# Performance work log

Measured on AMD Instinct MI355X. Metric: run time of the kernel, lower is better.

## Reference

```python
import jax, jax.numpy as jnp
import numpy as np
from jax import lax

ALPHA = float(np.exp(-1.0 / 5.0))   # exp(-1/tau_mem), tau_mem=5.0
THRESHOLD = 1.0


def _dwconv(x, w, b, groups):
    # x: (B, Cin, T), w: (Cout, Cin/groups, K), 'same' padding for odd K
    pad = (w.shape[-1] - 1) // 2
    y = lax.conv_general_dilated(
        x, w, window_strides=(1,), padding=[(pad, pad)],
        dimension_numbers=("NCH", "OIH", "NCH"), feature_group_count=groups)
    return y + b[None, :, None]


def setup_inputs() -> dict:
    key = jax.random.key(0)
    ks = jax.random.split(key, 12)
    B, C, T = 8, 256, 4096
    OP = 6            # out_per_kernel for each of the 3 kernel sizes
    DEC = 128         # decoder_channels
    f32 = jnp.float32
    d = {}
    d["x"] = jax.random.normal(ks[0], (B, C, T), f32)
    # depthwise multi-path conv params (groups=C): weight (C*OP, 1, K)
    d["w3"] = jax.random.normal(ks[1], (C * OP, 1, 3), f32) * 0.2
    d["b3"] = jnp.zeros((C * OP,), f32)
    d["w5"] = jax.random.normal(ks[2], (C * OP, 1, 5), f32) * 0.15
    d["b5"] = jnp.zeros((C * OP,), f32)
    d["w9"] = jax.random.normal(ks[3], (C * OP, 1, 9), f32) * 0.1
    d["b9"] = jnp.zeros((C * OP,), f32)
    # reduce: Conv1d(C*18 -> C, k=1, groups=C): weight (C, 18, 1)
    d["w_red"] = jax.random.normal(ks[4], (C, 3 * OP, 1), f32) * 0.2
    d["b_red"] = jnp.zeros((C,), f32)
    d["latency_scale"] = jnp.asarray(5.0, f32)
    # output_gates: xavier uniform (C, C) with zero diagonal
    bound = float(np.sqrt(6.0 / (C + C)))
    og = jax.random.uniform(ks[5], (C, C), f32, -bound, bound)
    d["output_gates"] = og * (1.0 - jnp.eye(C, dtype=f32))
    d["bias"] = jnp.zeros((C,), f32)
    # post_mlp: Linear(C, DEC) -> ReLU -> Linear(DEC, C); stored as (in, out)
    d["W1"] = jax.random.normal(ks[6], (C, DEC), f32) * float(np.sqrt(2.0 / C))
    d["b1"] = jnp.zeros((DEC,), f32)
    d["W2"] = jax.random.normal(ks[7], (DEC, C), f32) * float(np.sqrt(2.0 / DEC))
    d["b2"] = jnp.zeros((C,), f32)
    return d


def reference(x, w3, b3, w5, b5, w9, b9, w_red, b_red,
              latency_scale, output_gates, bias, W1, b1, W2, b2):
    B, C, T = x.shape
    # DepthwiseMultiPathEncoder: 3 depthwise convs -> cat -> grouped 1x1 reduce
    o3 = _dwconv(x, w3, b3, C)
    o5 = _dwconv(x, w5, b5, C)
    o9 = _dwconv(x, w9, b9, C)
    cat = jnp.concatenate([o3, o5, o9], axis=1)      # (B, 18C, T)
    drive = _dwconv(cat, w_red, b_red, C)             # (B, C, T)
    # LIF membrane recurrence + first-spike latency (sequential over T)
    d_t = jnp.moveaxis(drive, 2, 0)                   # (T, B, C)
    def step(V, dt):
        V = ALPHA * V + (1.0 - ALPHA) * dt
        return V, V >= THRESHOLD
    _, crossed = lax.scan(step, jnp.zeros((B, C), x.dtype), d_t)  # (T, B, C) bool
    fired_any = crossed.any(axis=0)
    first_t = jnp.argmax(crossed, axis=0)             # first True index
    true_latency = jnp.where(fired_any, first_t, T).astype(x.dtype)  # (B, C)
    # latency -> activation -> gated mix -> MLP -> softplus, clamp [0, T]
    scale = jnp.maximum(latency_scale, 0.001)
    act = jnp.exp(-true_latency / scale)              # (B, C)
    mixed = act @ output_gates.T + bias[None, :]      # (B, C)
    h = jax.nn.relu(mixed @ W1 + b1)
    raw_pred = h @ W2 + b2
    pred_latency = jnp.clip(jax.nn.softplus(raw_pred), 0.0, float(T))
    return pred_latency, true_latency, act
```

## Files before the change

kernel.cpp:

```cpp
#include <hip/hip_runtime.h>
#include <math.h>

#define C_CH 256
#define T_LEN 4096


template <int K>
__device__ inline void fold_bundle(const float* __restrict__ wp,
                                   const float* __restrict__ bp,
                                   const float* __restrict__ wred6,
                                   int p0, float* __restrict__ w9,
                                   float& bacc, int& src)
{
    const int off = (9 - K) >> 1;
    src = p0 / 6;
    #pragma unroll
    for (int k = 0; k < 9; ++k) w9[k] = 0.0f;
    #pragma unroll
    for (int j = 0; j < 6; ++j) {
        const float wr = wred6[j];
        bacc += wr * bp[p0 + j];
        #pragma unroll
        for (int k = 0; k < K; ++k)
            w9[off + k] += wr * wp[(p0 + j) * K + k];
    }
}

__global__ __launch_bounds__(256) void fold_kernel(
    const float* __restrict__ w3, const float* __restrict__ b3,
    const float* __restrict__ w5, const float* __restrict__ b5,
    const float* __restrict__ w9, const float* __restrict__ b9,
    const float* __restrict__ w_red, const float* __restrict__ b_red,
    float* __restrict__ ws)
{
    const int c = threadIdx.x;
    float wf[3][9];
    int   src[3];
    float bacc = 0.0f;
    #pragma unroll
    for (int r = 0; r < 3; ++r) {
        const int q0 = 18 * c + 6 * r;
        const float* wred6 = w_red + c * 18 + 6 * r;
        if (q0 < 1536)      fold_bundle<3>(w3, b3, wred6, q0,        wf[r], bacc, src[r]);
        else if (q0 < 3072) fold_bundle<5>(w5, b5, wred6, q0 - 1536, wf[r], bacc, src[r]);
        else                fold_bundle<9>(w9, b9, wred6, q0 - 3072, wf[r], bacc, src[r]);
    }
    float* o = ws + c * 32;
    #pragma unroll
    for (int r = 0; r < 3; ++r)
        #pragma unroll
        for (int k = 0; k < 9; ++k) o[r * 9 + k] = wf[r][k];
    o[27] = b_red[c] + bacc;
    #pragma unroll
    for (int r = 0; r < 3; ++r) ((int*)o)[28 + r] = src[r];
    o[31] = 0.0f;
}

__global__ __launch_bounds__(256) void drive_scan_kernel(
    const float* __restrict__ x,
    const float* __restrict__ ws,
    const float* __restrict__ latency_scale,
    float* __restrict__ out_lat, float* __restrict__ out_act)
{
    const int blk  = blockIdx.x;
    const int b    = blk >> 8;
    const int c    = blk & 255;
    const int tid  = threadIdx.x;
    const int lane = tid & 63;
    const int wv   = tid >> 6;

    __shared__ float sWS[32];
    __shared__ float sWaveTot[4];
    __shared__ float sCarry[4];
    __shared__ int   sMin[4];

    if (tid < 32) sWS[tid] = ws[c * 32 + tid];
    __syncthreads();

    const float A   = (float)0.8187307530779818;
    const float OMA = (float)(1.0 - 0.8187307530779818);
    const float Beff = sWS[27];

    float d[16];
    #pragma unroll
    for (int tt = 0; tt < 16; ++tt) d[tt] = Beff;

    const int i    = tid;
    const int base = 16 * i - 4;
    #pragma unroll
    for (int r = 0; r < 3; ++r) {
        const int srcc = ((const int*)sWS)[28 + r];
        const float* xr = x + ((size_t)b * C_CH + srcc) * T_LEN;
        float xa[24];
        if (i > 0 && i < 255) {
            const float4* p = (const float4*)(xr + base);
            #pragma unroll
            for (int v = 0; v < 6; ++v) {
                float4 q = p[v];
                xa[4 * v + 0] = q.x; xa[4 * v + 1] = q.y;
                xa[4 * v + 2] = q.z; xa[4 * v + 3] = q.w;
            }
        } else {
            #pragma unroll
            for (int e = 0; e < 24; ++e) {
                const int t = base + e;
                xa[e] = (t >= 0 && t < T_LEN) ? xr[t] : 0.0f;
            }
        }
        float wk[9];
        #pragma unroll
        for (int k = 0; k < 9; ++k) wk[k] = sWS[r * 9 + k];
        #pragma unroll
        for (int tt = 0; tt < 16; ++tt) {
            #pragma unroll
            for (int k = 0; k < 9; ++k)
                d[tt] = fmaf(wk[k], xa[tt + k], d[tt]);
        }
    }

    float S = 0.0f;
    #pragma unroll
    for (int tt = 0; tt < 16; ++tt) S = A * S + OMA * d[tt];

    const float Fp[6] = {
        (float)4.0762203978366215e-02,
        (float)1.6615572731739337e-03,
        (float)2.7607725720371943e-06,
        (float)7.6218649302532563e-12,
        (float)5.8092835977683129e-23,
        (float)3.3744728758705166e-45
    };
    float cinc = S;
    #pragma unroll
    for (int s = 0; s < 6; ++s) {
        const int o = 1 << s;
        const float y = __shfl_up(cinc, o, 64);
        if (lane >= o) cinc = fmaf(Fp[s], y, cinc);
    }
    if (lane == 63) sWaveTot[wv] = cinc;
    __syncthreads();
    if (tid == 0) {
        float g = 0.0f;
        #pragma unroll
        for (int w = 0; w < 4; ++w) { sCarry[w] = g; g = sWaveTot[w]; }
    }
    __syncthreads();
    const float cprev = __shfl_up(cinc, 1, 64);
    const float Vin = (lane ? cprev : 0.0f)
                    + expf(-3.2f * (float)lane) * sCarry[wv];

    float V = Vin;
    int firstT = T_LEN;
    #pragma unroll
    for (int tt = 0; tt < 16; ++tt) {
        V = A * V + OMA * d[tt];
        if (V >= 1.0f && firstT == T_LEN) firstT = 16 * i + tt;
    }

    #pragma unroll
    for (int o = 32; o > 0; o >>= 1)
        firstT = min(firstT, __shfl_xor(firstT, o, 64));
    if (lane == 0) sMin[wv] = firstT;
    __syncthreads();
    if (tid == 0) {
        const int f = min(min(sMin[0], sMin[1]), min(sMin[2], sMin[3]));
        const float lat   = (float)f;
        const float scale = fmaxf(latency_scale[0], 0.001f);
        out_lat[blk] = lat;
        out_act[blk] = expf(-lat / scale);
    }
}

__global__ __launch_bounds__(256) void mlp_kernel(
    const float* __restrict__ act,
    const float* __restrict__ og, const float* __restrict__ bias,
    const float* __restrict__ W1, const float* __restrict__ b1,
    const float* __restrict__ W2, const float* __restrict__ b2,
    float* __restrict__ out_pred)
{
    const int b = blockIdx.x;
    const int j = threadIdx.x;
    __shared__ float sAct[256];
    __shared__ float sMix[256];
    __shared__ float sH[128];

    sAct[j] = act[b * 256 + j];
    __syncthreads();

    float acc = bias[j];
    const float* ogr = og + (size_t)j * 256;
    for (int i2 = 0; i2 < 256; ++i2) acc = fmaf(sAct[i2], ogr[i2], acc);
    sMix[j] = acc;
    __syncthreads();

    if (j < 128) {
        float h = b1[j];
        for (int i2 = 0; i2 < 256; ++i2) h = fmaf(sMix[i2], W1[i2 * 128 + j], h);
        sH[j] = fmaxf(h, 0.0f);
    }
    __syncthreads();

    float raw = b2[j];
    for (int k = 0; k < 128; ++k) raw = fmaf(sH[k], W2[k * 256 + j], raw);

    const float sp = fmaxf(raw, 0.0f) + log1pf(expf(-fabsf(raw)));
    out_pred[b * 256 + j] = fminf(fmaxf(sp, 0.0f), 4096.0f);
}

extern "C" void kernel_launch(void* const* d_in, const int* in_sizes, int n_in,
                              void* d_out, int out_size, void* d_ws, size_t ws_size,
                              hipStream_t stream) {
    const float* x    = (const float*)d_in[0];
    const float* w3   = (const float*)d_in[1];
    const float* b3   = (const float*)d_in[2];
    const float* w5   = (const float*)d_in[3];
    const float* b5   = (const float*)d_in[4];
    const float* w9   = (const float*)d_in[5];
    const float* b9   = (const float*)d_in[6];
    const float* wred = (const float*)d_in[7];
    const float* bred = (const float*)d_in[8];
    const float* ls   = (const float*)d_in[9];
    const float* og   = (const float*)d_in[10];
    const float* bias = (const float*)d_in[11];
    const float* W1   = (const float*)d_in[12];
    const float* b1   = (const float*)d_in[13];
    const float* W2   = (const float*)d_in[14];
    const float* b2   = (const float*)d_in[15];

    float* ws       = (float*)d_ws;
    float* out      = (float*)d_out;
    float* out_pred = out;
    float* out_lat  = out + 2048;
    float* out_act  = out + 4096;

    fold_kernel<<<1, 256, 0, stream>>>(w3, b3, w5, b5, w9, b9, wred, bred, ws);
    drive_scan_kernel<<<2048, 256, 0, stream>>>(x, ws, ls, out_lat, out_act);
    mlp_kernel<<<8, 256, 0, stream>>>(out_act, og, bias, W1, b1, W2, b2, out_pred);
}
```

Baseline: 140.0 us.

## Fuse MLP tail into scan kernel via last-block atomic counter

Merges the separate MLP kernel into the drive/scan kernel: each block increments a global counter after writing its activation, and the last block to finish runs the gated mix and MLP for all 8 batches, with the weight loads shared across the batch. Source channel indices are now computed arithmetically instead of read from the workspace, all three x rows are loaded up front rather than per path, and weights are read straight from global memory instead of staged in shared memory. This removes one kernel launch and exposes more loads at once. In exchange the tail runs serially on a single block, register pressure rises from holding 72 x values, and correctness depends on the counter being reset by the fold kernel on every call.

New measurement: 201.8 us. 44.2% more time.

```diff
diff --git a/kernel.cpp b/kernel.cpp
--- a/kernel.cpp
+++ b/kernel.cpp
@@ -9,11 +9,9 @@
 __device__ inline void fold_bundle(const float* __restrict__ wp,
                                    const float* __restrict__ bp,
                                    const float* __restrict__ wred6,
-                                   int p0, float* __restrict__ w9,
-                                   float& bacc, int& src)
+                                   int p0, float* __restrict__ w9, float& bacc)
 {
     const int off = (9 - K) >> 1;
-    src = p0 / 6;
     #pragma unroll
     for (int k = 0; k < 9; ++k) w9[k] = 0.0f;
     #pragma unroll
@@ -35,15 +33,14 @@
 {
     const int c = threadIdx.x;
     float wf[3][9];
-    int   src[3];
     float bacc = 0.0f;
     #pragma unroll
     for (int r = 0; r < 3; ++r) {
         const int q0 = 18 * c + 6 * r;
         const float* wred6 = w_red + c * 18 + 6 * r;
-        if (q0 < 1536)      fold_bundle<3>(w3, b3, wred6, q0,        wf[r], bacc, src[r]);
-        else if (q0 < 3072) fold_bundle<5>(w5, b5, wred6, q0 - 1536, wf[r], bacc, src[r]);
-        else                fold_bundle<9>(w9, b9, wred6, q0 - 3072, wf[r], bacc, src[r]);
+        if (q0 < 1536)      fold_bundle<3>(w3, b3, wred6, q0,        wf[r], bacc);
+        else if (q0 < 3072) fold_bundle<5>(w5, b5, wred6, q0 - 1536, wf[r], bacc);
+        else                fold_bundle<9>(w9, b9, wred6, q0 - 3072, wf[r], bacc);
     }
     float* o = ws + c * 32;
     #pragma unroll
@@ -51,16 +48,18 @@
         #pragma unroll
         for (int k = 0; k < 9; ++k) o[r * 9 + k] = wf[r][k];
     o[27] = b_red[c] + bacc;
-    #pragma unroll
-    for (int r = 0; r < 3; ++r) ((int*)o)[28 + r] = src[r];
-    o[31] = 0.0f;
-}
-
-__global__ __launch_bounds__(256) void drive_scan_kernel(
-    const float* __restrict__ x,
-    const float* __restrict__ ws,
+    o[28] = 0.0f; o[29] = 0.0f; o[30] = 0.0f; o[31] = 0.0f;
+    if (c == 0) ((int*)ws)[8192] = 0;
+}
+
+__global__ __launch_bounds__(256) void fused_kernel(
+    const float* __restrict__ x, const float* __restrict__ ws,
     const float* __restrict__ latency_scale,
-    float* __restrict__ out_lat, float* __restrict__ out_act)
+    const float* __restrict__ og, const float* __restrict__ bias,
+    const float* __restrict__ W1, const float* __restrict__ b1,
+    const float* __restrict__ W2, const float* __restrict__ b2,
+    float* __restrict__ out_pred, float* __restrict__ out_lat,
+    float* __restrict__ out_act, int* __restrict__ counter)
 {
     const int blk  = blockIdx.x;
     const int b    = blk >> 8;
@@ -69,54 +68,54 @@
     const int lane = tid & 63;
     const int wv   = tid >> 6;
 
-    __shared__ float sWS[32];
     __shared__ float sWaveTot[4];
     __shared__ float sCarry[4];
     __shared__ int   sMin[4];
-
-    if (tid < 32) sWS[tid] = ws[c * 32 + tid];
-    __syncthreads();
+    __shared__ int   sIsLast;
+
+    const int base = 16 * tid - 4;
+    float xa[3][24];
+    #pragma unroll
+    for (int r = 0; r < 3; ++r) {
+        const int q      = 18 * c + 6 * r;
+        const int region = (q >= 1536) + (q >= 3072);
+        const int srcc   = 3 * c + r - (region << 8);
+        const float* xr  = x + ((size_t)b * C_CH + srcc) * T_LEN;
+        if (tid > 0 && tid < 255) {
+            const float4* p = (const float4*)(xr + base);
+            #pragma unroll
+            for (int v = 0; v < 6; ++v) {
+                float4 q4 = p[v];
+                xa[r][4 * v + 0] = q4.x; xa[r][4 * v + 1] = q4.y;
+                xa[r][4 * v + 2] = q4.z; xa[r][4 * v + 3] = q4.w;
+            }
+        } else {
+            #pragma unroll
+            for (int e = 0; e < 24; ++e) {
+                const int t = base + e;
+                xa[r][e] = (t >= 0 && t < T_LEN) ? xr[t] : 0.0f;
+            }
+        }
+    }
+
+    const float* wc = ws + c * 32;
+    const float Beff = wc[27];
+    float d[16];
+    #pragma unroll
+    for (int tt = 0; tt < 16; ++tt) d[tt] = Beff;
+    #pragma unroll
+    for (int r = 0; r < 3; ++r) {
+        #pragma unroll
+        for (int k = 0; k < 9; ++k) {
+            const float wk = wc[r * 9 + k];
+            #pragma unroll
+            for (int tt = 0; tt < 16; ++tt)
+                d[tt] = fmaf(wk, xa[r][tt + k], d[tt]);
+        }
+    }
 
     const float A   = (float)0.8187307530779818;
     const float OMA = (float)(1.0 - 0.8187307530779818);
-    const float Beff = sWS[27];
-
-    float d[16];
-    #pragma unroll
-    for (int tt = 0; tt < 16; ++tt) d[tt] = Beff;
-
-    const int i    = tid;
-    const int base = 16 * i - 4;
-    #pragma unroll
-    for (int r = 0; r < 3; ++r) {
-        const int srcc = ((const int*)sWS)[28 + r];
-        const float* xr = x + ((size_t)b * C_CH + srcc) * T_LEN;
-        float xa[24];
-        if (i > 0 && i < 255) {
-            const float4* p = (const float4*)(xr + base);
-            #pragma unroll
-            for (int v = 0; v < 6; ++v) {
-                float4 q = p[v];
-                xa[4 * v + 0] = q.x; xa[4 * v + 1] = q.y;
-                xa[4 * v + 2] = q.z; xa[4 * v + 3] = q.w;
-            }
-        } else {
-            #pragma unroll
-            for (int e = 0; e < 24; ++e) {
-                const int t = base + e;
-                xa[e] = (t >= 0 && t < T_LEN) ? xr[t] : 0.0f;
-            }
-        }
-        float wk[9];
-        #pragma unroll
-        for (int k = 0; k < 9; ++k) wk[k] = sWS[r * 9 + k];
-        #pragma unroll
-        for (int tt = 0; tt < 16; ++tt) {
-            #pragma unroll
-            for (int k = 0; k < 9; ++k)
-                d[tt] = fmaf(wk[k], xa[tt + k], d[tt]);
-        }
-    }
 
     float S = 0.0f;
     #pragma unroll
@@ -154,7 +153,7 @@
     #pragma unroll
     for (int tt = 0; tt < 16; ++tt) {
         V = A * V + OMA * d[tt];
-        if (V >= 1.0f && firstT == T_LEN) firstT = 16 * i + tt;
+        if (V >= 1.0f && firstT == T_LEN) firstT = 16 * tid + tt;
     }
 
     #pragma unroll
@@ -168,43 +167,69 @@
         const float scale = fmaxf(latency_scale[0], 0.001f);
         out_lat[blk] = lat;
         out_act[blk] = expf(-lat / scale);
-    }
-}
-
-__global__ __launch_bounds__(256) void mlp_kernel(
-    const float* __restrict__ act,
-    const float* __restrict__ og, const float* __restrict__ bias,
-    const float* __restrict__ W1, const float* __restrict__ b1,
-    const float* __restrict__ W2, const float* __restrict__ b2,
-    float* __restrict__ out_pred)
-{
-    const int b = blockIdx.x;
-    const int j = threadIdx.x;
-    __shared__ float sAct[256];
-    __shared__ float sMix[256];
-    __shared__ float sH[128];
-
-    sAct[j] = act[b * 256 + j];
-    __syncthreads();
-
-    float acc = bias[j];
-    const float* ogr = og + (size_t)j * 256;
-    for (int i2 = 0; i2 < 256; ++i2) acc = fmaf(sAct[i2], ogr[i2], acc);
-    sMix[j] = acc;
+        __threadfence();
+        const int old = atomicAdd(counter, 1);
+        sIsLast = (old == 2047) ? 1 : 0;
+    }
+    __syncthreads();
+    if (!sIsLast) return;
+
+    __threadfence();
+    __shared__ float sAct[2048];
+    __shared__ float sMix[2048];
+    __shared__ float sH[1024];
+    for (int t = tid; t < 2048; t += 256) sAct[t] = out_act[t];
+    __syncthreads();
+
+    const int j = tid;
+    {
+        float mix[8];
+        #pragma unroll
+        for (int bb = 0; bb < 8; ++bb) mix[bb] = bias[j];
+        const float* ogr = og + (size_t)j * 256;
+        for (int i = 0; i < 256; ++i) {
+            const float w = ogr[i];
+            #pragma unroll
+            for (int bb = 0; bb < 8; ++bb)
+                mix[bb] = fmaf(sAct[bb * 256 + i], w, mix[bb]);
+        }
+        #pragma unroll
+        for (int bb = 0; bb < 8; ++bb) sMix[bb * 256 + j] = mix[bb];
+    }
     __syncthreads();
 
     if (j < 128) {
-        float h = b1[j];
-        for (int i2 = 0; i2 < 256; ++i2) h = fmaf(sMix[i2], W1[i2 * 128 + j], h);
-        sH[j] = fmaxf(h, 0.0f);
-    }
-    __syncthreads();
-
-    float raw = b2[j];
-    for (int k = 0; k < 128; ++k) raw = fmaf(sH[k], W2[k * 256 + j], raw);
-
-    const float sp = fmaxf(raw, 0.0f) + log1pf(expf(-fabsf(raw)));
-    out_pred[b * 256 + j] = fminf(fmaxf(sp, 0.0f), 4096.0f);
+        float h[8];
+        #pragma unroll
+        for (int bb = 0; bb < 8; ++bb) h[bb] = b1[j];
+        for (int i = 0; i < 256; ++i) {
+            const float w = W1[i * 128 + j];
+            #pragma unroll
+            for (int bb = 0; bb < 8; ++bb)
+                h[bb] = fmaf(sMix[bb * 256 + i], w, h[bb]);
+        }
+        #pragma unroll
+        for (int bb = 0; bb < 8; ++bb) sH[bb * 128 + j] = fmaxf(h[bb], 0.0f);
+    }
+    __syncthreads();
+
+    {
+        float raw[8];
+        #pragma unroll
+        for (int bb = 0; bb < 8; ++bb) raw[bb] = b2[j];
+        for (int k = 0; k < 128; ++k) {
+            const float w = W2[k * 256 + j];
+            #pragma unroll
+            for (int bb = 0; bb < 8; ++bb)
+                raw[bb] = fmaf(sH[bb * 128 + k], w, raw[bb]);
+        }
+        #pragma unroll
+        for (int bb = 0; bb < 8; ++bb) {
+            const float r = raw[bb];
+            const float sp = fmaxf(r, 0.0f) + log1pf(expf(-fabsf(r)));
+            out_pred[bb * 256 + j] = fminf(fmaxf(sp, 0.0f), 4096.0f);
+        }
+    }
 }
 
 extern "C" void kernel_launch(void* const* d_in, const int* in_sizes, int n_in,
@@ -228,12 +253,13 @@
     const float* b2   = (const float*)d_in[15];
 
     float* ws       = (float*)d_ws;
+    int*   counter  = ((int*)d_ws) + 8192;
     float* out      = (float*)d_out;
     float* out_pred = out;
     float* out_lat  = out + 2048;
     float* out_act  = out + 4096;
 
     fold_kernel<<<1, 256, 0, stream>>>(w3, b3, w5, b5, w9, b9, wred, bred, ws);
-    drive_scan_kernel<<<2048, 256, 0, stream>>>(x, ws, ls, out_lat, out_act);
-    mlp_kernel<<<8, 256, 0, stream>>>(out_act, og, bias, W1, b1, W2, b2, out_pred);
-}
+    fused_kernel<<<2048, 256, 0, stream>>>(x, ws, ls, og, bias, W1, b1, W2, b2,
+                                           out_pred, out_lat, out_act, counter);
+}
```
